# Optimization experiments

Measured on AMD Instinct MI355X. Metric: run time of the kernel, lower is better.

## Reference

```python
import jax, jax.numpy as jnp
import numpy as np

# FCHL19 representation (Christensen et al., JCP 2020), as implemented by
# QMLightning's pairlist_gpu/egto_gpu/fchl_gpu CUDA kernels, re-expressed as
# dense masked pair/triplet tensors (non-periodic: cell/inv_cell empty).
SPECIES = np.array([1.0, 6.0, 7.0, 8.0], dtype=np.float32)
NSPEC = 4
NRS2 = 24
NRS3 = 20
RCUT = 8.0
ETA2 = 0.32
ETA3 = 2.7
TWO_BODY_DECAY = 1.8
THREE_BODY_DECAY = 0.57
THREE_BODY_WEIGHT = float(np.sqrt(ETA3 / np.pi) * 13.4)  # module pre-scales weight
RS2 = np.linspace(0.0, RCUT, NRS2 + 1)[1:].astype(np.float32)
RS3 = np.linspace(0.0, RCUT, NRS3 + 1)[1:].astype(np.float32)
NPAIR = NSPEC * (NSPEC + 1) // 2  # unordered species pairs -> 10

def _pair_map():
    M = np.zeros((NSPEC, NSPEC, NPAIR), np.float32)
    i = 0
    for p in range(NSPEC):
        for q in range(p, NSPEC):
            M[p, q, i] = 1.0
            M[q, p, i] = 1.0
            i += 1
    return M
PAIR_MAP = _pair_map()

B_MOL, MAX_ATOMS = 64, 28


def setup_inputs() -> dict:
    key = jax.random.key(0)
    k1, k2, k3 = jax.random.split(key, 3)
    X = jax.random.uniform(k1, (B_MOL, MAX_ATOMS, 3), jnp.float32) * 6.0
    atom_counts = jax.random.randint(k2, (B_MOL,), 24, MAX_ATOMS + 1).astype(jnp.int32)
    zidx = jax.random.randint(k3, (B_MOL, MAX_ATOMS), 0, NSPEC)
    valid = jnp.arange(MAX_ATOMS)[None, :] < atom_counts[:, None]
    Z = jnp.where(valid, jnp.asarray(SPECIES)[zidx], 0.0).astype(jnp.float32)
    atomIDs = jnp.arange(B_MOL * MAX_ATOMS, dtype=jnp.int32)
    molIDs = jnp.repeat(jnp.arange(B_MOL, dtype=jnp.int32), MAX_ATOMS)
    return {"X": X, "Z": Z, "atomIDs": atomIDs, "molIDs": molIDs, "atom_counts": atom_counts}


def _fchl(X, Z, atom_counts):
    B, N, _ = X.shape
    valid = jnp.arange(N)[None, :] < atom_counts[:, None]               # [B,N]
    diff = X[:, :, None, :] - X[:, None, :, :]                          # [B,N,N,3]
    d2 = jnp.sum(diff * diff, -1)
    eye = jnp.eye(N, dtype=bool)[None]
    pair_ok = valid[:, :, None] & valid[:, None, :] & (~eye)
    r = jnp.sqrt(jnp.where(pair_ok, d2, 1.0))                           # grad-safe distances
    within = pair_ok & (r < RCUT)
    fc = jnp.where(within, 0.5 * (jnp.cos(jnp.pi * r / RCUT) + 1.0), 0.0)
    oh = (Z[:, :, None] == jnp.asarray(SPECIES)[None, None, :]).astype(X.dtype)  # [B,N,S]

    # --- two-body: log-normal radial expansion, 1/r^decay scaling, cosine cutoff ---
    ln = jnp.log1p(ETA2 / (r * r))                                      # sigma^2
    mu = jnp.log(r) - 0.5 * ln
    rs2 = jnp.asarray(RS2)
    norm = 1.0 / (jnp.sqrt(ln)[..., None] * np.float32(np.sqrt(2.0 * np.pi)) * rs2)
    radial2 = (fc / jnp.power(r, TWO_BODY_DECAY))[..., None] * norm * \
        jnp.exp(-(jnp.log(rs2) - mu[..., None]) ** 2 / (2.0 * ln[..., None]))     # [B,N,N,M]
    rep2 = jnp.einsum('bijm,bjs->bism', radial2, oh).reshape(B, N, NSPEC * NRS2)

    # --- three-body: Axilrod-Teller-weighted radial x Fourier(order 1) angular ---
    rij = r[:, :, :, None]   # [B,i,j,1] -> broadcast over k
    rik = r[:, :, None, :]
    rjk = r[:, None, :, :]
    triu = (jnp.arange(N)[:, None] < jnp.arange(N)[None, :])[None, None]  # j<k
    m3 = within[:, :, :, None] & within[:, :, None, :] & triu
    rjk_s = jnp.where(m3, rjk, 1.0)
    cos_i = jnp.where(m3, (rij**2 + rik**2 - rjk_s**2) / (2.0 * rij * rik), 0.0)
    cos_j = (rij**2 + rjk_s**2 - rik**2) / (2.0 * rij * rjk_s)
    cos_k = (rik**2 + rjk_s**2 - rij**2) / (2.0 * rik * rjk_s)
    atm = (1.0 + 3.0 * cos_i * cos_j * cos_k) / jnp.power(rij * rik * rjk_s, THREE_BODY_DECAY)
    w = jnp.where(m3, THREE_BODY_WEIGHT * atm * fc[:, :, :, None] * fc[:, :, None, :], 0.0)
    c = jnp.clip(cos_i, -1.0, 1.0)
    s = jnp.sqrt(jnp.clip(1.0 - c * c, 1e-12, 1.0))
    ang = jnp.stack([2.0 * c, 2.0 * s], -1) * w[..., None]              # [B,N,N,N,2]
    radial3 = jnp.exp(-ETA3 * (0.5 * (rij + rik)[..., None] - jnp.asarray(RS3)) ** 2)  # [B,N,N,N,L]
    pair_oh = jnp.einsum('bjp,bkq,pqP->bjkP', oh, oh, jnp.asarray(PAIR_MAP))           # [B,N,N,10]
    t = jnp.einsum('bijka,bjkP->bijkaP', ang, pair_oh)
    rep3 = jnp.einsum('bijkaP,bijkl->biPla', t, radial3).reshape(B, N, NPAIR * NRS3 * 2)

    return jnp.concatenate([rep2, rep3], -1)  # [B,N,496]


def reference(X, Z, atomIDs, molIDs, atom_counts):
    # atomIDs/molIDs are CUDA block-assignment bookkeeping; math doesn't use them.
    return _fchl(X, Z, atom_counts)
```

## Files before the change

kernel.cpp:

```cpp
#include <hip/hip_runtime.h>

#define B_MOL 64
#define MAXN 28
#define NSPEC 4
#define NRS2 24
#define NRS3 20
#define NPAIR 10
#define NCOMB 378
#define SPAIR_CAP 408
#define REP2_LEN (NSPEC * NRS2)
#define REP3_LEN (NPAIR * NRS3 * 2)
#define OUT_LEN (REP2_LEN + REP3_LEN)
#define NBIN3 (NPAIR * NRS3)
#define RCUT 8.0f
#define ETA2 0.32f
#define ETA3 2.7f
#define LOG2E 1.4426950408889634f
#define LN2F 0.6931471805599453f
#define W3 12.4225783348083f

#define PAD4(c) (((c) + 3) & ~3)

__device__ __forceinline__ float hexp2(float x) { return __builtin_amdgcn_exp2f(x); }
__device__ __forceinline__ float hlog2(float x) { return __builtin_amdgcn_logf(x); }
__device__ __forceinline__ float hrcp(float x)  { return __builtin_amdgcn_rcpf(x); }
__device__ __forceinline__ float hrsq(float x)  { return __builtin_amdgcn_rsqf(x); }
__device__ __forceinline__ float hcos_rev(float t) { return __builtin_amdgcn_cosf(t); }

struct PairTab { unsigned short jk[NCOMB]; };
static constexpr PairTab make_tab() {
    PairTab t{};
    int idx = 0;
    for (int j = 0; j < MAXN; ++j)
        for (int k = j + 1; k < MAXN; ++k)
            t.jk[idx++] = (unsigned short)((j << 8) | k);
    return t;
}
__constant__ PairTab PT = make_tab();

__global__ __launch_bounds__(256) void fchl_kernel(
    const float* __restrict__ X,
    const float* __restrict__ Z,
    const int* __restrict__ counts,
    float* __restrict__ out)
{
    const int i = blockIdx.x;
    const int b = blockIdx.y;
    const int tid = threadIdx.x;
    const int cnt = counts[b];

    __shared__ float sx[MAXN], sy[MAXN], szc[MAXN];
    __shared__ int   s_win[MAXN];
    __shared__ float s_r[MAXN], s_fc[MAXN];
    __shared__ float s_mu[MAXN + 1], s_i2ln[MAXN + 1], s_pref[MAXN + 1];
    __shared__ int   sspec[MAXN];
    __shared__ int   cntP[NPAIR], curP[NPAIR];
    __shared__ int   cntSp[NSPEC];
    __shared__ int   spList[NSPEC][32];
    __shared__ signed char s_tag[NCOMB];
    __shared__ float4 s_pair[SPAIR_CAP];

    float* orow = out + (size_t)(b * MAXN + i) * OUT_LEN;

    {
        const float4 z4 = make_float4(0.f, 0.f, 0.f, 0.f);
        for (int t = tid; t < SPAIR_CAP; t += 256) s_pair[t] = z4;
    }
    if (tid >= 28 && tid < 28 + NSPEC) cntSp[tid - 28] = 0;
    if (tid >= 64 && tid < 64 + NPAIR) { cntP[tid - 64] = 0; curP[tid - 64] = 0; }
    if (tid == MAXN) { s_pref[MAXN] = 0.f; s_mu[MAXN] = 0.f; s_i2ln[MAXN] = 1.f; }
    if (tid < MAXN) {
        const int j = tid;
        float xi = X[(b * MAXN + i) * 3 + 0];
        float yi = X[(b * MAXN + i) * 3 + 1];
        float zi = X[(b * MAXN + i) * 3 + 2];
        float xj = X[(b * MAXN + j) * 3 + 0];
        float yj = X[(b * MAXN + j) * 3 + 1];
        float zj = X[(b * MAXN + j) * 3 + 2];
        sx[j] = xj; sy[j] = yj; szc[j] = zj;
        float z = Z[b * MAXN + j];
        int s = -1;
        if (z == 1.0f) s = 0;
        else if (z == 6.0f) s = 1;
        else if (z == 7.0f) s = 2;
        else if (z == 8.0f) s = 3;
        sspec[j] = s;

        float dx = xi - xj, dy = yi - yj, dz = zi - zj;
        float r = sqrtf(dx * dx + dy * dy + dz * dz);
        bool w = (i < cnt) && (j < cnt) && (j != i) && (r < RCUT);
        s_win[j] = w ? 1 : 0;
        if (w) {
            float fc = 0.5f * (hcos_rev(r * (1.0f / 16.0f)) + 1.0f);
            float ln = LN2F * hlog2(1.0f + ETA2 * hrcp(r * r));
            float lr = LN2F * hlog2(r);
            s_r[j] = r;
            s_fc[j] = fc;
            s_mu[j] = lr - 0.5f * ln;
            s_i2ln[j] = LOG2E / (2.0f * ln);
            s_pref[j] = fc * hexp2(-1.8f * hlog2(r)) * hrsq(ln);
            int pos = atomicAdd(&cntSp[s], 1);
            spList[s][pos] = j;
        } else {
            s_r[j] = 1.0f; s_fc[j] = 0.0f; s_mu[j] = 0.0f;
            s_i2ln[j] = 1.0f; s_pref[j] = 0.0f;
        }
    }
    __syncthreads();

    for (int idx = tid; idx < NCOMB; idx += 256) {
        int jk = PT.jk[idx];
        int j = jk >> 8, k = jk & 255;
        int tg = -1;
        if (s_win[j] && s_win[k]) {
            int pj = sspec[j], pk = sspec[k];
            int pp = min(pj, pk), q = max(pj, pk);
            tg = pp * NSPEC - (pp * (pp - 1)) / 2 + (q - pp);
            atomicAdd(&cntP[tg], 1);
        }
        s_tag[idx] = (signed char)tg;
    }
    __syncthreads();

    for (int idx = tid; idx < NCOMB; idx += 256) {
        int tg = s_tag[idx];
        if (tg < 0) continue;
        int jk = PT.jk[idx];
        int j = jk >> 8, k = jk & 255;

        float rij = s_r[j], rik = s_r[k];
        float dx = sx[j] - sx[k], dy = sy[j] - sy[k], dz = szc[j] - szc[k];
        float rjk = sqrtf(dx * dx + dy * dy + dz * dz);

        float rij2 = rij * rij, rik2 = rik * rik, rjk2 = rjk * rjk;
        float cos_i = (rij2 + rik2 - rjk2) * 0.5f * hrcp(rij * rik);
        float cos_j = (rij2 + rjk2 - rik2) * 0.5f * hrcp(rij * rjk);
        float cos_k = (rik2 + rjk2 - rij2) * 0.5f * hrcp(rik * rjk);

        float atm = (1.0f + 3.0f * cos_i * cos_j * cos_k)
                    * hexp2(-0.57f * hlog2(rij * rik * rjk));
        float w = W3 * atm * s_fc[j] * s_fc[k];

        float c = fminf(fmaxf(cos_i, -1.0f), 1.0f);
        float sn = sqrtf(fminf(fmaxf(1.0f - c * c, 1e-12f), 1.0f));

        int bs = 0;
        #pragma unroll
        for (int q = 0; q < NPAIR - 1; ++q) bs += (q < tg) ? PAD4(cntP[q]) : 0;
        int slot = bs + atomicAdd(&curP[tg], 1);
        s_pair[slot] = make_float4(0.5f * (rij + rik), 2.0f * c * w, 2.0f * sn * w, 0.0f);
    }
    __syncthreads();

    if (tid < NBIN3) {
        const int P = tid / NRS3;
        const int l = tid % NRS3;
        const float rs = 0.4f * (float)(l + 1);
        int s0 = 0;
        #pragma unroll
        for (int q = 0; q < NPAIR - 1; ++q) s0 += (q < P) ? PAD4(cntP[q]) : 0;
        const int trip = PAD4(cntP[P]);
        float acc0 = 0.0f, acc1 = 0.0f;
        for (int s = s0; s < s0 + trip; s += 4) {
            float4 p0 = s_pair[s + 0];
            float4 p1 = s_pair[s + 1];
            float4 p2 = s_pair[s + 2];
            float4 p3 = s_pair[s + 3];
            float d0 = p0.x - rs, d1 = p1.x - rs, d2 = p2.x - rs, d3 = p3.x - rs;
            float e0 = hexp2(-(ETA3 * LOG2E) * d0 * d0);
            float e1 = hexp2(-(ETA3 * LOG2E) * d1 * d1);
            float e2 = hexp2(-(ETA3 * LOG2E) * d2 * d2);
            float e3 = hexp2(-(ETA3 * LOG2E) * d3 * d3);
            acc0 += p0.y * e0 + p1.y * e1 + p2.y * e2 + p3.y * e3;
            acc1 += p0.z * e0 + p1.z * e1 + p2.z * e2 + p3.z * e3;
        }
        orow[REP2_LEN + P * (NRS3 * 2) + l * 2 + 0] = acc0;
        orow[REP2_LEN + P * (NRS3 * 2) + l * 2 + 1] = acc1;
    } else {
        for (int t2 = tid - 200; t2 < REP2_LEN; t2 += 56) {
            const int sp = t2 / NRS2;
            const int m = t2 % NRS2;
            const float rs2 = (float)(m + 1) * (8.0f / 24.0f);
            const float lrs2 = LN2F * hlog2(rs2);
            const float nrm = 0.3989422804014327f / rs2;
            const int n = cntSp[sp];
            const int trip = PAD4(n);
            float acc = 0.0f;
            for (int c = 0; c < trip; c += 4) {
                int r0 = spList[sp][c + 0];
                int r1 = spList[sp][c + 1];
                int r2 = spList[sp][c + 2];
                int r3 = spList[sp][c + 3];
                int j0 = (c + 0 < n) ? r0 : MAXN;
                int j1 = (c + 1 < n) ? r1 : MAXN;
                int j2 = (c + 2 < n) ? r2 : MAXN;
                int j3 = (c + 3 < n) ? r3 : MAXN;
                float d0 = lrs2 - s_mu[j0], d1 = lrs2 - s_mu[j1];
                float d2 = lrs2 - s_mu[j2], d3 = lrs2 - s_mu[j3];
                acc += s_pref[j0] * hexp2(-d0 * d0 * s_i2ln[j0])
                     + s_pref[j1] * hexp2(-d1 * d1 * s_i2ln[j1])
                     + s_pref[j2] * hexp2(-d2 * d2 * s_i2ln[j2])
                     + s_pref[j3] * hexp2(-d3 * d3 * s_i2ln[j3]);
            }
            orow[sp * NRS2 + m] = acc * nrm;
        }
    }
}

extern "C" void kernel_launch(void* const* d_in, const int* in_sizes, int n_in,
                              void* d_out, int out_size, void* d_ws, size_t ws_size,
                              hipStream_t stream) {
    const float* X = (const float*)d_in[0];
    const float* Z = (const float*)d_in[1];
    const int* counts = (const int*)d_in[4];
    float* out = (float*)d_out;

    dim3 grid(MAXN, B_MOL);
    dim3 block(256);
    hipLaunchKernelGGL(fchl_kernel, grid, block, 0, stream, X, Z, counts, out);
}
```

Before: 18.06 us.

## Process seven center atoms per block and drop per-species neighbor lists

Each block now handles a batch of 7 center atoms of one molecule, so the grid shrinks from 1792 blocks to 256 and molecule coordinates and species are loaded once per block. Per-atom shared arrays gain a batch dimension, and the triplet and output loops are flattened over the batch to keep all 256 threads busy. The two-body term now loops over all 28 neighbors with a species mask instead of building atomic per-species lists. The costs are about 7x more shared memory per block, which lowers occupancy, and fewer blocks than the GPU has compute units.

Measured after the change: 36.91 us. 2.04x slower.

```diff
diff --git a/kernel.cpp b/kernel.cpp
--- a/kernel.cpp
+++ b/kernel.cpp
@@ -2,6 +2,8 @@
 
 #define B_MOL 64
 #define MAXN 28
+#define BATCH 7
+#define NGRP 4
 #define NSPEC 4
 #define NRS2 24
 #define NRS3 20
@@ -44,40 +46,32 @@
     const int* __restrict__ counts,
     float* __restrict__ out)
 {
-    const int i = blockIdx.x;
-    const int b = blockIdx.y;
+    const int blk = blockIdx.x;
+    const int b  = blk >> 2;
+    const int i0 = (blk & 3) * BATCH;
     const int tid = threadIdx.x;
     const int cnt = counts[b];
 
-    __shared__ float sx[MAXN], sy[MAXN], szc[MAXN];
-    __shared__ int   s_win[MAXN];
-    __shared__ float s_r[MAXN], s_fc[MAXN];
-    __shared__ float s_mu[MAXN + 1], s_i2ln[MAXN + 1], s_pref[MAXN + 1];
+    __shared__ float s_xyz[MAXN * 3];
     __shared__ int   sspec[MAXN];
-    __shared__ int   cntP[NPAIR], curP[NPAIR];
-    __shared__ int   cntSp[NSPEC];
-    __shared__ int   spList[NSPEC][32];
-    __shared__ signed char s_tag[NCOMB];
-    __shared__ float4 s_pair[SPAIR_CAP];
-
-    float* orow = out + (size_t)(b * MAXN + i) * OUT_LEN;
+    __shared__ unsigned char s_win[BATCH][MAXN];
+    __shared__ float s_rm[BATCH][MAXN], s_fcm[BATCH][MAXN];
+    __shared__ float s_mu[BATCH][MAXN], s_i2[BATCH][MAXN], s_pf[BATCH][MAXN];
+    __shared__ int   cntP[BATCH][NPAIR], curP[BATCH][NPAIR];
+    __shared__ signed char s_tag[BATCH][NCOMB];
+    __shared__ float4 s_pair[BATCH][SPAIR_CAP];
 
     {
         const float4 z4 = make_float4(0.f, 0.f, 0.f, 0.f);
-        for (int t = tid; t < SPAIR_CAP; t += 256) s_pair[t] = z4;
-    }
-    if (tid >= 28 && tid < 28 + NSPEC) cntSp[tid - 28] = 0;
-    if (tid >= 64 && tid < 64 + NPAIR) { cntP[tid - 64] = 0; curP[tid - 64] = 0; }
-    if (tid == MAXN) { s_pref[MAXN] = 0.f; s_mu[MAXN] = 0.f; s_i2ln[MAXN] = 1.f; }
-    if (tid < MAXN) {
-        const int j = tid;
-        float xi = X[(b * MAXN + i) * 3 + 0];
-        float yi = X[(b * MAXN + i) * 3 + 1];
-        float zi = X[(b * MAXN + i) * 3 + 2];
-        float xj = X[(b * MAXN + j) * 3 + 0];
-        float yj = X[(b * MAXN + j) * 3 + 1];
-        float zj = X[(b * MAXN + j) * 3 + 2];
-        sx[j] = xj; sy[j] = yj; szc[j] = zj;
+        float4* sp = &s_pair[0][0];
+        for (int t = tid; t < BATCH * SPAIR_CAP; t += 256) sp[t] = z4;
+        int* cp = &cntP[0][0];
+        int* up = &curP[0][0];
+        for (int t = tid; t < BATCH * NPAIR; t += 256) { cp[t] = 0; up[t] = 0; }
+    }
+    if (tid < MAXN * 3) s_xyz[tid] = X[b * (MAXN * 3) + tid];
+    if (tid >= 196 && tid < 196 + MAXN) {
+        int j = tid - 196;
         float z = Z[b * MAXN + j];
         int s = -1;
         if (z == 1.0f) s = 0;
@@ -85,51 +79,62 @@
         else if (z == 7.0f) s = 2;
         else if (z == 8.0f) s = 3;
         sspec[j] = s;
-
+    }
+    if (tid < BATCH * MAXN) {
+        const int a = tid / MAXN;
+        const int j = tid - a * MAXN;
+        const int i = i0 + a;
+        const float* Xb = X + b * (MAXN * 3);
+        float xi = Xb[i * 3 + 0], yi = Xb[i * 3 + 1], zi = Xb[i * 3 + 2];
+        float xj = Xb[j * 3 + 0], yj = Xb[j * 3 + 1], zj = Xb[j * 3 + 2];
         float dx = xi - xj, dy = yi - yj, dz = zi - zj;
         float r = sqrtf(dx * dx + dy * dy + dz * dz);
         bool w = (i < cnt) && (j < cnt) && (j != i) && (r < RCUT);
-        s_win[j] = w ? 1 : 0;
+        s_win[a][j] = w ? 1 : 0;
         if (w) {
             float fc = 0.5f * (hcos_rev(r * (1.0f / 16.0f)) + 1.0f);
             float ln = LN2F * hlog2(1.0f + ETA2 * hrcp(r * r));
             float lr = LN2F * hlog2(r);
-            s_r[j] = r;
-            s_fc[j] = fc;
-            s_mu[j] = lr - 0.5f * ln;
-            s_i2ln[j] = LOG2E / (2.0f * ln);
-            s_pref[j] = fc * hexp2(-1.8f * hlog2(r)) * hrsq(ln);
-            int pos = atomicAdd(&cntSp[s], 1);
-            spList[s][pos] = j;
+            s_rm[a][j] = r;
+            s_fcm[a][j] = fc;
+            s_mu[a][j] = lr - 0.5f * ln;
+            s_i2[a][j] = LOG2E / (2.0f * ln);
+            s_pf[a][j] = fc * hexp2(-1.8f * hlog2(r)) * hrsq(ln);
         } else {
-            s_r[j] = 1.0f; s_fc[j] = 0.0f; s_mu[j] = 0.0f;
-            s_i2ln[j] = 1.0f; s_pref[j] = 0.0f;
+            s_rm[a][j] = 1.0f; s_fcm[a][j] = 0.0f; s_mu[a][j] = 0.0f;
+            s_i2[a][j] = 1.0f; s_pf[a][j] = 0.0f;
         }
     }
     __syncthreads();
 
-    for (int idx = tid; idx < NCOMB; idx += 256) {
+    for (int t = tid; t < BATCH * NCOMB; t += 256) {
+        int a = t / NCOMB;
+        int idx = t - a * NCOMB;
         int jk = PT.jk[idx];
         int j = jk >> 8, k = jk & 255;
         int tg = -1;
-        if (s_win[j] && s_win[k]) {
+        if (s_win[a][j] && s_win[a][k]) {
             int pj = sspec[j], pk = sspec[k];
             int pp = min(pj, pk), q = max(pj, pk);
             tg = pp * NSPEC - (pp * (pp - 1)) / 2 + (q - pp);
-            atomicAdd(&cntP[tg], 1);
+            atomicAdd(&cntP[a][tg], 1);
         }
-        s_tag[idx] = (signed char)tg;
+        s_tag[a][idx] = (signed char)tg;
     }
     __syncthreads();
 
-    for (int idx = tid; idx < NCOMB; idx += 256) {
-        int tg = s_tag[idx];
+    for (int t = tid; t < BATCH * NCOMB; t += 256) {
+        int a = t / NCOMB;
+        int idx = t - a * NCOMB;
+        int tg = s_tag[a][idx];
         if (tg < 0) continue;
         int jk = PT.jk[idx];
         int j = jk >> 8, k = jk & 255;
 
-        float rij = s_r[j], rik = s_r[k];
-        float dx = sx[j] - sx[k], dy = sy[j] - sy[k], dz = szc[j] - szc[k];
+        float rij = s_rm[a][j], rik = s_rm[a][k];
+        float dx = s_xyz[j * 3 + 0] - s_xyz[k * 3 + 0];
+        float dy = s_xyz[j * 3 + 1] - s_xyz[k * 3 + 1];
+        float dz = s_xyz[j * 3 + 2] - s_xyz[k * 3 + 2];
         float rjk = sqrtf(dx * dx + dy * dy + dz * dz);
 
         float rij2 = rij * rij, rik2 = rik * rik, rjk2 = rjk * rjk;
@@ -139,69 +144,64 @@
 
         float atm = (1.0f + 3.0f * cos_i * cos_j * cos_k)
                     * hexp2(-0.57f * hlog2(rij * rik * rjk));
-        float w = W3 * atm * s_fc[j] * s_fc[k];
+        float w = W3 * atm * s_fcm[a][j] * s_fcm[a][k];
 
         float c = fminf(fmaxf(cos_i, -1.0f), 1.0f);
         float sn = sqrtf(fminf(fmaxf(1.0f - c * c, 1e-12f), 1.0f));
 
         int bs = 0;
         #pragma unroll
-        for (int q = 0; q < NPAIR - 1; ++q) bs += (q < tg) ? PAD4(cntP[q]) : 0;
-        int slot = bs + atomicAdd(&curP[tg], 1);
-        s_pair[slot] = make_float4(0.5f * (rij + rik), 2.0f * c * w, 2.0f * sn * w, 0.0f);
+        for (int q = 0; q < NPAIR - 1; ++q) bs += (q < tg) ? PAD4(cntP[a][q]) : 0;
+        int slot = bs + atomicAdd(&curP[a][tg], 1);
+        s_pair[a][slot] = make_float4(0.5f * (rij + rik), 2.0f * c * w, 2.0f * sn * w, 0.0f);
     }
     __syncthreads();
 
-    if (tid < NBIN3) {
-        const int P = tid / NRS3;
-        const int l = tid % NRS3;
-        const float rs = 0.4f * (float)(l + 1);
-        int s0 = 0;
-        #pragma unroll
-        for (int q = 0; q < NPAIR - 1; ++q) s0 += (q < P) ? PAD4(cntP[q]) : 0;
-        const int trip = PAD4(cntP[P]);
-        float acc0 = 0.0f, acc1 = 0.0f;
-        for (int s = s0; s < s0 + trip; s += 4) {
-            float4 p0 = s_pair[s + 0];
-            float4 p1 = s_pair[s + 1];
-            float4 p2 = s_pair[s + 2];
-            float4 p3 = s_pair[s + 3];
-            float d0 = p0.x - rs, d1 = p1.x - rs, d2 = p2.x - rs, d3 = p3.x - rs;
-            float e0 = hexp2(-(ETA3 * LOG2E) * d0 * d0);
-            float e1 = hexp2(-(ETA3 * LOG2E) * d1 * d1);
-            float e2 = hexp2(-(ETA3 * LOG2E) * d2 * d2);
-            float e3 = hexp2(-(ETA3 * LOG2E) * d3 * d3);
-            acc0 += p0.y * e0 + p1.y * e1 + p2.y * e2 + p3.y * e3;
-            acc1 += p0.z * e0 + p1.z * e1 + p2.z * e2 + p3.z * e3;
-        }
-        orow[REP2_LEN + P * (NRS3 * 2) + l * 2 + 0] = acc0;
-        orow[REP2_LEN + P * (NRS3 * 2) + l * 2 + 1] = acc1;
-    } else {
-        for (int t2 = tid - 200; t2 < REP2_LEN; t2 += 56) {
-            const int sp = t2 / NRS2;
-            const int m = t2 % NRS2;
+    const int base_atom = b * MAXN + i0;
+    for (int t = tid; t < BATCH * (NBIN3 + REP2_LEN); t += 256) {
+        if (t < BATCH * NBIN3) {
+            int a = t / NBIN3;
+            int rem = t - a * NBIN3;
+            int P = rem / NRS3, l = rem - P * NRS3;
+            const float rs = 0.4f * (float)(l + 1);
+            int s0 = 0;
+            #pragma unroll
+            for (int q = 0; q < NPAIR - 1; ++q) s0 += (q < P) ? PAD4(cntP[a][q]) : 0;
+            const int trip = PAD4(cntP[a][P]);
+            float acc0 = 0.0f, acc1 = 0.0f;
+            const float4* row = s_pair[a];
+            for (int s = s0; s < s0 + trip; s += 4) {
+                float4 p0 = row[s + 0];
+                float4 p1 = row[s + 1];
+                float4 p2 = row[s + 2];
+                float4 p3 = row[s + 3];
+                float d0 = p0.x - rs, d1 = p1.x - rs, d2 = p2.x - rs, d3 = p3.x - rs;
+                float e0 = hexp2(-(ETA3 * LOG2E) * d0 * d0);
+                float e1 = hexp2(-(ETA3 * LOG2E) * d1 * d1);
+                float e2 = hexp2(-(ETA3 * LOG2E) * d2 * d2);
+                float e3 = hexp2(-(ETA3 * LOG2E) * d3 * d3);
+                acc0 += p0.y * e0 + p1.y * e1 + p2.y * e2 + p3.y * e3;
+                acc1 += p0.z * e0 + p1.z * e1 + p2.z * e2 + p3.z * e3;
+            }
+            float* orow = out + (size_t)(base_atom + a) * OUT_LEN;
+            orow[REP2_LEN + P * (NRS3 * 2) + l * 2 + 0] = acc0;
+            orow[REP2_LEN + P * (NRS3 * 2) + l * 2 + 1] = acc1;
+        } else {
+            int t2 = t - BATCH * NBIN3;
+            int a = t2 / REP2_LEN;
+            int rem = t2 - a * REP2_LEN;
+            int sp = rem / NRS2, m = rem - sp * NRS2;
             const float rs2 = (float)(m + 1) * (8.0f / 24.0f);
             const float lrs2 = LN2F * hlog2(rs2);
             const float nrm = 0.3989422804014327f / rs2;
-            const int n = cntSp[sp];
-            const int trip = PAD4(n);
             float acc = 0.0f;
-            for (int c = 0; c < trip; c += 4) {
-                int r0 = spList[sp][c + 0];
-                int r1 = spList[sp][c + 1];
-                int r2 = spList[sp][c + 2];
-                int r3 = spList[sp][c + 3];
-                int j0 = (c + 0 < n) ? r0 : MAXN;
-                int j1 = (c + 1 < n) ? r1 : MAXN;
-                int j2 = (c + 2 < n) ? r2 : MAXN;
-                int j3 = (c + 3 < n) ? r3 : MAXN;
-                float d0 = lrs2 - s_mu[j0], d1 = lrs2 - s_mu[j1];
-                float d2 = lrs2 - s_mu[j2], d3 = lrs2 - s_mu[j3];
-                acc += s_pref[j0] * hexp2(-d0 * d0 * s_i2ln[j0])
-                     + s_pref[j1] * hexp2(-d1 * d1 * s_i2ln[j1])
-                     + s_pref[j2] * hexp2(-d2 * d2 * s_i2ln[j2])
-                     + s_pref[j3] * hexp2(-d3 * d3 * s_i2ln[j3]);
+            #pragma unroll 4
+            for (int j = 0; j < MAXN; ++j) {
+                float d = lrs2 - s_mu[a][j];
+                float v = s_pf[a][j] * hexp2(-d * d * s_i2[a][j]);
+                acc += (sspec[j] == sp) ? v : 0.0f;
             }
+            float* orow = out + (size_t)(base_atom + a) * OUT_LEN;
             orow[sp * NRS2 + m] = acc * nrm;
         }
     }
@@ -215,7 +215,7 @@
     const int* counts = (const int*)d_in[4];
     float* out = (float*)d_out;
 
-    dim3 grid(MAXN, B_MOL);
+    dim3 grid(B_MOL * NGRP);
     dim3 block(256);
     hipLaunchKernelGGL(fchl_kernel, grid, block, 0, stream, X, Z, counts, out);
 }
```
